# Kernel tuning notes

Measured on AMD Instinct MI355X. Metric: run time of the kernel, lower is better.

## Reference

```python
import jax, jax.numpy as jnp
import numpy as np

D = 192      # model dim (out_channels)
DIN = 384    # d_inner = 2*D
N = 16       # d_state
DTR = 12     # dt_rank = ceil(D/16)
K = 4        # depthwise conv kernel size
NB = 3       # total mamba blocks (2 stacked + 1 in downsample)


def setup_inputs() -> dict:
    key = jax.random.key(0)
    ks = jax.random.split(key, 8)
    rn = lambda k, shape, s: jax.random.normal(k, shape, jnp.float32) * s
    inp = {
        "x": jax.random.normal(ks[0], (2, 96, 56, 56), jnp.float32),
        "proj_w": rn(ks[1], (D, 96), 0.1),
        "proj_b": jnp.zeros((D,), jnp.float32),
        "bn_g": jnp.ones((D,), jnp.float32),
        "bn_b": jnp.zeros((D,), jnp.float32),
        "bn_mean": jnp.zeros((D,), jnp.float32),
        "bn_var": jnp.ones((D,), jnp.float32),
        "ln_g": jnp.ones((NB, D), jnp.float32),
        "ln_b": jnp.zeros((NB, D), jnp.float32),
        "Win": rn(ks[2], (NB, 2 * DIN, D), 0.05),
        "b_in": jnp.zeros((NB, 2 * DIN), jnp.float32),
        "conv_w": rn(ks[3], (NB, DIN, K), 0.2),
        "conv_b": jnp.zeros((NB, DIN), jnp.float32),
        "Wx": rn(ks[4], (NB, DTR + 2 * N, DIN), 0.05),
        "Wdt": rn(ks[5], (NB, DIN, DTR), 0.05),
        "bdt": jnp.full((NB, DIN), -4.6, jnp.float32),  # softplus ~ 0.01
        "A_log": jnp.log(jnp.broadcast_to(jnp.arange(1, N + 1, dtype=jnp.float32), (NB, DIN, N))),
        "Dskip": jnp.ones((NB, DIN), jnp.float32),
        "Wout": rn(ks[6], (NB, D, DIN), 0.05),
        "bout": jnp.zeros((NB, D), jnp.float32),
    }
    return inp


def _mamba(x, ln_g, ln_b, Win, b_in, conv_w, conv_b, Wx, Wdt, bdt, A_log, Dskip, Wout, bout):
    # x: (B, C, H, W) -> flatten spatial dims to a sequence (B, L, C)
    B, C, H, W = x.shape
    L = H * W
    seq = x.reshape(B, C, L).transpose(0, 2, 1)
    mu = seq.mean(-1, keepdims=True)
    var = seq.var(-1, keepdims=True)
    h = (seq - mu) * jax.lax.rsqrt(var + 1e-5) * ln_g + ln_b  # LayerNorm
    xz = jnp.einsum('bld,ed->ble', h, Win) + b_in              # (B, L, 2*DIN)
    xi, z = jnp.split(xz, 2, axis=-1)
    # depthwise causal conv1d along L
    xc = jnp.pad(xi.transpose(0, 2, 1), ((0, 0), (0, 0), (K - 1, 0)))
    xc = jax.lax.conv_general_dilated(xc, conv_w[:, None, :], (1,), 'VALID',
                                      feature_group_count=DIN) + conv_b[:, None]
    xi = jax.nn.silu(xc).transpose(0, 2, 1)                    # (B, L, DIN)
    proj = jnp.einsum('ble,pe->blp', xi, Wx)                   # (B, L, DTR+2N)
    dtl = proj[..., :DTR]
    Bm = proj[..., DTR:DTR + N]
    Cm = proj[..., DTR + N:]
    dt = jax.nn.softplus(jnp.einsum('blr,er->ble', dtl, Wdt) + bdt)  # (B, L, DIN)
    A = -jnp.exp(A_log)                                         # (DIN, N)
    dA = jnp.exp(dt[..., None] * A)                             # (B, L, DIN, N)
    dBx = (dt * xi)[..., None] * Bm[:, :, None, :]              # (B, L, DIN, N)

    def step(hc, t):
        dA_t, dBx_t, C_t = t
        hc = dA_t * hc + dBx_t                                  # (B, DIN, N)
        return hc, jnp.einsum('ben,bn->be', hc, C_t)

    h0 = jnp.zeros((B, DIN, N), x.dtype)
    _, ys = jax.lax.scan(step, h0, (dA.transpose(1, 0, 2, 3),
                                    dBx.transpose(1, 0, 2, 3),
                                    Cm.transpose(1, 0, 2)))
    y = ys.transpose(1, 0, 2) + Dskip * xi
    y = y * jax.nn.silu(z)
    out = jnp.einsum('ble,de->bld', y, Wout) + bout
    return out.transpose(0, 2, 1).reshape(B, C, H, W)


def _maxpool2(x):
    return jax.lax.reduce_window(x, -jnp.inf, jax.lax.max,
                                 (1, 1, 2, 2), (1, 1, 2, 2), 'VALID')


def reference(x, proj_w, proj_b, bn_g, bn_b, bn_mean, bn_var, ln_g, ln_b, Win, b_in,
              conv_w, conv_b, Wx, Wdt, bdt, A_log, Dskip, Wout, bout):
    # proj (conv1x1) + BatchNorm (eval-mode running stats)
    x = jnp.einsum('bchw,oc->bohw', x, proj_w) + proj_b[:, None, None]
    x = (x - bn_mean[:, None, None]) * jax.lax.rsqrt(bn_var[:, None, None] + 1e-5) \
        * bn_g[:, None, None] + bn_b[:, None, None]
    blk = lambda i, v: _mamba(v, ln_g[i], ln_b[i], Win[i], b_in[i], conv_w[i], conv_b[i],
                              Wx[i], Wdt[i], bdt[i], A_log[i], Dskip[i], Wout[i], bout[i])
    for i in range(2):  # residual mamba blocks
        x = x + blk(i, x)
    skip = x
    x = blk(2, _maxpool2(x))  # downsample: maxpool then mamba (no residual)
    return (x, skip)
```

## Files before the change

### kernel.cpp

```cpp
#include <hip/hip_runtime.h>

typedef __attribute__((ext_vector_type(8))) __bf16 bf16x8;
typedef __attribute__((ext_vector_type(4))) __bf16 bf16x4;
typedef __attribute__((ext_vector_type(4))) float f32x4;

#define DEV static __device__ __forceinline__

DEV float fast_rcp(float x) { return __builtin_amdgcn_rcpf(x); }
DEV float sigm(float x) { return fast_rcp(1.f + __expf(-x)); }
DEV float siluf(float x) { return x * sigm(x); }
DEV float softplusf(float x) { return x > 20.f ? x : __logf(1.f + __expf(x)); }


__global__ __launch_bounds__(256) void k_proj_wcvt(
    const float* __restrict__ x, const float* __restrict__ pw,
    const float* __restrict__ pb, const float* __restrict__ bng,
    const float* __restrict__ bnb, const float* __restrict__ bnm,
    const float* __restrict__ bnv, float* __restrict__ v,
    const float* __restrict__ Win, const float* __restrict__ Wout,
    const float* __restrict__ Wx, __bf16* __restrict__ Wb)
{
  constexpr int SAP = 104;
  __shared__ __bf16 As[64 * SAP];
  __shared__ __bf16 Ws[64 * SAP];
  const int tid = threadIdx.x;
  const int bid = blockIdx.x;

  if (bid >= 294) {
    const int idx = ((bid - 294) * 256 + tid) * 4;
    if (idx < 714240) {
      const float* src;
      if (idx < 442368) src = Win + idx;
      else if (idx < 663552) src = Wout + (idx - 442368);
      else src = Wx + (idx - 663552);
      const float4 tv = *(const float4*)src;
      bf16x4 o;
      o[0] = (__bf16)tv.x; o[1] = (__bf16)tv.y;
      o[2] = (__bf16)tv.z; o[3] = (__bf16)tv.w;
      *(bf16x4*)(Wb + idx) = o;
    }
    return;
  }

  const int r0 = (bid % 98) * 64;
  const int col0 = (bid / 98) * 64;
  const int b = r0 / 3136, l0 = r0 % 3136;
  const int lane = tid & 63, wv = tid >> 6;
  const int rh = wv >> 1, ch = wv & 1;
  const int lm = lane & 15, quad = lane >> 4;

#pragma unroll
  for (int it = 0; it < 6; ++it) {
    const int idx = tid + it * 256;
    const int c = idx >> 4, l4 = idx & 15;
    const float4 t = *(const float4*)(x + ((size_t)(b * 96 + c)) * 3136 + l0 + l4 * 4);
    As[(l4 * 4 + 0) * SAP + c] = (__bf16)t.x;
    As[(l4 * 4 + 1) * SAP + c] = (__bf16)t.y;
    As[(l4 * 4 + 2) * SAP + c] = (__bf16)t.z;
    As[(l4 * 4 + 3) * SAP + c] = (__bf16)t.w;
  }
#pragma unroll
  for (int it = 0; it < 6; ++it) {
    const int idx = tid + it * 256;
    const int wr = idx / 24, kc = (idx % 24) * 4;
    const float4 t = *(const float4*)(pw + (size_t)(col0 + wr) * 96 + kc);
    bf16x4 o;
    o[0] = (__bf16)t.x; o[1] = (__bf16)t.y; o[2] = (__bf16)t.z; o[3] = (__bf16)t.w;
    *(bf16x4*)(&Ws[wr * SAP + kc]) = o;
  }
  __syncthreads();

  f32x4 acc[2][2] = {};
#pragma unroll
  for (int ks = 0; ks < 3; ++ks) {
    const int kb = ks * 32 + quad * 8;
    bf16x8 a0 = *(const bf16x8*)(&As[(rh * 32 + lm) * SAP + kb]);
    bf16x8 a1 = *(const bf16x8*)(&As[(rh * 32 + 16 + lm) * SAP + kb]);
    bf16x8 b0 = *(const bf16x8*)(&Ws[(ch * 32 + lm) * SAP + kb]);
    bf16x8 b1 = *(const bf16x8*)(&Ws[(ch * 32 + 16 + lm) * SAP + kb]);
    acc[0][0] = __builtin_amdgcn_mfma_f32_16x16x32_bf16(a0, b0, acc[0][0], 0, 0, 0);
    acc[0][1] = __builtin_amdgcn_mfma_f32_16x16x32_bf16(a0, b1, acc[0][1], 0, 0, 0);
    acc[1][0] = __builtin_amdgcn_mfma_f32_16x16x32_bf16(a1, b0, acc[1][0], 0, 0, 0);
    acc[1][1] = __builtin_amdgcn_mfma_f32_16x16x32_bf16(a1, b1, acc[1][1], 0, 0, 0);
  }

#pragma unroll
  for (int ti = 0; ti < 2; ++ti)
#pragma unroll
    for (int tj = 0; tj < 2; ++tj) {
      const int gcol = col0 + ch * 32 + tj * 16 + lm;
      const float s = rsqrtf(bnv[gcol] + 1e-5f) * bng[gcol];
      const float sh = (pb[gcol] - bnm[gcol]) * s + bnb[gcol];
#pragma unroll
      for (int j = 0; j < 4; ++j) {
        const int grow = r0 + rh * 32 + ti * 16 + quad * 4 + j;
        v[(size_t)grow * 192 + gcol] = acc[ti][tj][j] * s + sh;
      }
    }
}

__global__ __launch_bounds__(256) void k_conv(
    const float* __restrict__ xz, __bf16* __restrict__ xiB,
    const float* __restrict__ cw, const float* __restrict__ cb,
    int Lseq, int nthreads)
{
  const int idx = blockIdx.x * 256 + threadIdx.x;
  if (idx >= nthreads) return;
  const int e = idx % 384;
  const int seg = idx / 384;
  const int nseg = Lseq / 8;
  const int b = seg / nseg;
  const int l0 = (seg % nseg) * 8;
  const float4 w4 = *(const float4*)(cw + e * 4);
  const float bv = cb[e];
  float xv[11];
#pragma unroll
  for (int k = 0; k < 11; ++k) {
    const int l = l0 - 3 + k;
    xv[k] = (l >= 0) ? xz[(size_t)(b * Lseq + l) * 768 + e] : 0.f;
  }
#pragma unroll
  for (int j = 0; j < 8; ++j) {
    const float a = bv + xv[j] * w4.x + xv[j + 1] * w4.y + xv[j + 2] * w4.z + xv[j + 3] * w4.w;
    xiB[(size_t)(b * Lseq + l0 + j) * 384 + e] = (__bf16)siluf(a);
  }
}

template <int AMODE>
__global__ __launch_bounds__(256, 4) void k_gemm_xz(
    const float* __restrict__ A, const __bf16* __restrict__ W,
    const float* __restrict__ bias, float* __restrict__ O,
    int M, const float* __restrict__ lng, const float* __restrict__ lnb)
{
  constexpr int SA = 200;
  __shared__ __bf16 As[64 * SA];
  __shared__ float lnS[384];
  const int tid = threadIdx.x;
  const int r0 = blockIdx.x * 64;
  const int col0 = blockIdx.y * 128;
  const int lane = tid & 63, wv = tid >> 6;
  const int rh = wv & 1, ch = wv >> 1;
  const int lm = lane & 15, quad = lane >> 4;

  if (tid < 192) { lnS[tid] = lng[tid]; lnS[192 + tid] = lnb[tid]; }
  __syncthreads();

  {
    const int row = tid >> 2, part = tid & 3;
    const int gr = min(r0 + row, M - 1);
    const int cbase = part * 48;
    float4 tv[12];
    if constexpr (AMODE == 2) {
#pragma unroll
      for (int j = 0; j < 12; ++j)
        tv[j] = *(const float4*)(A + (size_t)gr * 192 + cbase + j * 4);
    } else {
      const int bb = gr / 784, l2 = gr % 784;
      const int h2 = l2 / 28, w2 = l2 % 28;
      const float* p0 = A + (size_t)(bb * 3136 + h2 * 112 + w2 * 2) * 192;
#pragma unroll
      for (int j = 0; j < 12; ++j) {
        const int cc = cbase + j * 4;
        const float4 a0 = *(const float4*)(p0 + cc);
        const float4 a1 = *(const float4*)(p0 + 192 + cc);
        const float4 a2 = *(const float4*)(p0 + 56 * 192 + cc);
        const float4 a3 = *(const float4*)(p0 + 57 * 192 + cc);
        tv[j].x = fmaxf(fmaxf(a0.x, a1.x), fmaxf(a2.x, a3.x));
        tv[j].y = fmaxf(fmaxf(a0.y, a1.y), fmaxf(a2.y, a3.y));
        tv[j].z = fmaxf(fmaxf(a0.z, a1.z), fmaxf(a2.z, a3.z));
        tv[j].w = fmaxf(fmaxf(a0.w, a1.w), fmaxf(a2.w, a3.w));
      }
    }
    float s = 0.f, sq = 0.f;
#pragma unroll
    for (int j = 0; j < 12; ++j) {
      s += tv[j].x + tv[j].y + tv[j].z + tv[j].w;
      sq += tv[j].x * tv[j].x + tv[j].y * tv[j].y + tv[j].z * tv[j].z + tv[j].w * tv[j].w;
    }
    s += __shfl_xor(s, 1); s += __shfl_xor(s, 2);
    sq += __shfl_xor(sq, 1); sq += __shfl_xor(sq, 2);
    const float mean = s * (1.f / 192.f);
    const float rstd = rsqrtf(sq * (1.f / 192.f) - mean * mean + 1e-5f);
#pragma unroll
    for (int j = 0; j < 12; ++j) {
      const int c = cbase + j * 4;
      bf16x4 o;
      o[0] = (__bf16)((tv[j].x - mean) * rstd * lnS[c + 0] + lnS[192 + c + 0]);
      o[1] = (__bf16)((tv[j].y - mean) * rstd * lnS[c + 1] + lnS[192 + c + 1]);
      o[2] = (__bf16)((tv[j].z - mean) * rstd * lnS[c + 2] + lnS[192 + c + 2]);
      o[3] = (__bf16)((tv[j].w - mean) * rstd * lnS[c + 3] + lnS[192 + c + 3]);
      *(bf16x4*)(&As[row * SA + c]) = o;
    }
  }
  __syncthreads();

  f32x4 acc[2][4] = {};
#pragma unroll
  for (int ks = 0; ks < 6; ++ks) {
    const int kb = ks * 32 + quad * 8;
    bf16x8 a0 = *(const bf16x8*)(&As[(rh * 32 + lm) * SA + kb]);
    bf16x8 a1 = *(const bf16x8*)(&As[(rh * 32 + 16 + lm) * SA + kb]);
#pragma unroll
    for (int tj = 0; tj < 4; ++tj) {
      const int gw = col0 + ch * 64 + tj * 16 + lm;
      bf16x8 bfr = *(const bf16x8*)(W + (size_t)gw * 192 + kb);
      acc[0][tj] = __builtin_amdgcn_mfma_f32_16x16x32_bf16(a0, bfr, acc[0][tj], 0, 0, 0);
      acc[1][tj] = __builtin_amdgcn_mfma_f32_16x16x32_bf16(a1, bfr, acc[1][tj], 0, 0, 0);
    }
  }

#pragma unroll
  for (int ti = 0; ti < 2; ++ti)
#pragma unroll
    for (int tj = 0; tj < 4; ++tj) {
      const int gcol = col0 + ch * 64 + tj * 16 + lm;
      const float bv = bias[gcol];
#pragma unroll
      for (int j = 0; j < 4; ++j) {
        const int rowt = rh * 32 + ti * 16 + quad * 4 + j;
        const int grow = r0 + rowt;
        if (grow < M) O[(size_t)grow * 768 + gcol] = acc[ti][tj][j] + bv;
      }
    }
}

constexpr int EPI_G2 = 1, EPI_RES = 2, EPI_RES_SKIP = 3, EPI_OUT2 = 4;

template <int EPI>
__global__ __launch_bounds__(256) void k_gemm_s(
    const __bf16* __restrict__ Ab, const __bf16* __restrict__ W,
    const float* __restrict__ bias, float* __restrict__ O,
    int M, int K, int Nvalid,
    float* __restrict__ dtlbuf, float* __restrict__ bcbuf,
    float* __restrict__ oflt)
{
  constexpr int SA = 200;
  __shared__ __bf16 As[16 * SA];
  __shared__ float dtlS[(EPI == EPI_G2) ? 16 * 12 : 1];
  const int tid = threadIdx.x;
  const int r0 = blockIdx.x * 16;
  const int col0 = blockIdx.y * 64;
  const int lane = tid & 63, wv = tid >> 6;
  const int ch = wv;
  const int lm = lane & 15, quad = lane >> 4;

  f32x4 acc = {};
  const int nkp = K / 192;
  for (int kp = 0; kp < nkp; ++kp) {
    if (kp) __syncthreads();
    {
      const int idx = tid;
      const int row = idx / 24, kc = (idx % 24) * 8;
      const int gr = min(r0 + row, M - 1);
      if (row < 16)
        *(bf16x8*)(&As[row * SA + kc]) =
            *(const bf16x8*)(Ab + (size_t)gr * K + kp * 192 + kc);
      const int idx2 = tid + 256;
      if (idx2 < 384) {
        const int row2 = idx2 / 24, kc2 = (idx2 % 24) * 8;
        const int gr2 = min(r0 + row2, M - 1);
        *(bf16x8*)(&As[row2 * SA + kc2]) =
            *(const bf16x8*)(Ab + (size_t)gr2 * K + kp * 192 + kc2);
      }
    }
    __syncthreads();
#pragma unroll
    for (int ks = 0; ks < 6; ++ks) {
      const int kb = ks * 32 + quad * 8;
      bf16x8 a0 = *(const bf16x8*)(&As[lm * SA + kb]);
      const int gw = min(col0 + ch * 16 + lm, Nvalid - 1);
      bf16x8 bfr = *(const bf16x8*)(W + (size_t)gw * K + kp * 192 + kb);
      acc = __builtin_amdgcn_mfma_f32_16x16x32_bf16(a0, bfr, acc, 0, 0, 0);
    }
  }

  const int colt = ch * 16 + lm;
  if constexpr (EPI == EPI_G2) {
#pragma unroll
    for (int j = 0; j < 4; ++j) {
      const int rowt = quad * 4 + j;
      const int grow = r0 + rowt;
      const float val = acc[j];
      if (colt < 12) dtlS[rowt * 12 + colt] = val;
      else if (colt < 44 && grow < M)
        bcbuf[(size_t)grow * 32 + (colt - 12)] = val;
    }
    __syncthreads();
    if (tid < 192) {
      const int grow = r0 + tid / 12;
      if (grow < M) dtlbuf[(size_t)grow * 12 + tid % 12] = dtlS[tid];
    }
  } else {
    const int gcol = col0 + colt;
    const float bv = bias[gcol];
#pragma unroll
    for (int j = 0; j < 4; ++j) {
      const int rowt = quad * 4 + j;
      const int grow = r0 + rowt;
      if (grow >= M) continue;
      const float val = acc[j] + bv;
      if constexpr (EPI == EPI_RES) {
        O[(size_t)grow * 192 + gcol] += val;
      } else if constexpr (EPI == EPI_RES_SKIP) {
        const float nv = O[(size_t)grow * 192 + gcol] + val;
        O[(size_t)grow * 192 + gcol] = nv;
        const int b = grow / 3136, l = grow % 3136;
        oflt[b * 602112 + gcol * 3136 + l] = nv;
      } else {
        const int b = grow / 784, l = grow % 784;
        oflt[b * 150528 + gcol * 784 + l] = val;
      }
    }
  }
}

constexpr int SC_LC = 14, SC_T = 7, SC_TN = 2;

DEV void compute_dts(const float* __restrict__ dtl, const float* __restrict__ Wdt,
                     const float* __restrict__ bdt, int rowbase, int e, int t,
                     float* dtlS, float* wdtS)
{
  for (int idx = t; idx < SC_LC * 12; idx += 128)
    dtlS[idx] = dtl[(size_t)(rowbase + idx / 12) * 12 + idx % 12];
#pragma unroll
  for (int r = 0; r < 12; ++r) wdtS[r * 128 + t] = Wdt[(size_t)e * 12 + r];
}

__global__ __launch_bounds__(128) void k_scan1(
    const float* __restrict__ dtl, const __bf16* __restrict__ xi,
    const float* __restrict__ bc, const float* __restrict__ Wdt,
    const float* __restrict__ bdt, const float* __restrict__ A_log,
    float* __restrict__ DT, float* __restrict__ S, int Lseq, int NC)
{
  __shared__ float Bs[SC_LC * 16];
  __shared__ float dts[SC_LC * 128];
  __shared__ float dtlS[SC_LC * 12];
  __shared__ float wdtS[12 * 128];
  const int t = threadIdx.x;
  const int e = blockIdx.y * 128 + t;
  const int c = blockIdx.x % NC;
  const int b = blockIdx.x / NC;
  const int rowbase = b * Lseq + c * SC_LC;

  for (int idx = t; idx < SC_LC * 16; idx += 128) {
    const int l = idx >> 4, q = idx & 15;
    Bs[idx] = bc[(size_t)(rowbase + l) * 32 + q];
  }
  compute_dts(dtl, Wdt, bdt, rowbase, e, t, dtlS, wdtS);
  const float bdte = bdt[e];

  float An2[16];
  {
    const float4* a4 = (const float4*)(A_log + e * 16);
    float4 t0 = a4[0], t1 = a4[1], t2 = a4[2], t3 = a4[3];
    float tmp[16] = {t0.x, t0.y, t0.z, t0.w, t1.x, t1.y, t1.z, t1.w,
                     t2.x, t2.y, t2.z, t2.w, t3.x, t3.y, t3.z, t3.w};
#pragma unroll
    for (int n = 0; n < 16; ++n) An2[n] = -__expf(tmp[n]) * 1.44269504f;
  }
  __syncthreads();
  float dtsum = 0.f;
  for (int l = 0; l < SC_LC; ++l) {
    float a = bdte;
#pragma unroll
    for (int r = 0; r < 12; ++r) a += dtlS[l * 12 + r] * wdtS[r * 128 + t];
    const float sp = softplusf(a);
    dts[l * 128 + t] = sp;
    dtsum += sp;
  }

  float h[16];
#pragma unroll
  for (int n = 0; n < 16; ++n) h[n] = 0.f;

  float xA[SC_T], xB[SC_T];
  auto LOADA = [&](int tt) {
#pragma unroll
    for (int j = 0; j < SC_T; ++j)
      xA[j] = (float)xi[(size_t)(rowbase + tt * SC_T + j) * 384 + e];
  };
  auto LOADB = [&](int tt) {
#pragma unroll
    for (int j = 0; j < SC_T; ++j)
      xB[j] = (float)xi[(size_t)(rowbase + tt * SC_T + j) * 384 + e];
  };
  auto COMP = [&](const float (&x8)[SC_T], int tt) {
#pragma unroll
    for (int j = 0; j < SC_T; ++j) {
      const int l = tt * SC_T + j;
      const float dtv = dts[l * 128 + t];
      const float u = dtv * x8[j];
      const float* Brow = &Bs[l * 16];
#pragma unroll
      for (int n = 0; n < 16; ++n) {
        const float a = __builtin_amdgcn_exp2f(dtv * An2[n]);
        h[n] = a * h[n] + u * Brow[n];
      }
    }
  };

  LOADA(0);
#pragma unroll
  for (int tt = 0; tt < SC_TN; ++tt) {
    if (tt & 1) { if (tt + 1 < SC_TN) LOADA(tt + 1); COMP(xB, tt); }
    else        { if (tt + 1 < SC_TN) LOADB(tt + 1); COMP(xA, tt); }
  }

  const size_t o = ((size_t)(b * NC + c) * 384 + e) * 16;
#pragma unroll
  for (int q = 0; q < 4; ++q)
    *(float4*)(S + o + q * 4) = make_float4(h[q*4], h[q*4+1], h[q*4+2], h[q*4+3]);
  DT[(size_t)(b * NC + c) * 384 + e] = dtsum;
}

__global__ __launch_bounds__(256) void k_carry(
    const float* __restrict__ DT, float* __restrict__ SH,
    const float* __restrict__ A_log, int NC)
{
  const int tid = blockIdx.x * 256 + threadIdx.x;
  const int b = tid / 6144, r = tid % 6144;
  const float An2 = -__expf(A_log[r]) * 1.44269504f;
  const size_t o = (size_t)b * NC * 6144 + r;
  const size_t od = (size_t)b * NC * 384 + (r >> 4);

  float sA[8], dA[8], sB[8], dB[8];
  auto LOAD = [&](float (&sv)[8], float (&dv)[8], int c0) {
#pragma unroll
    for (int k = 0; k < 8; ++k) {
      sv[k] = SH[o + (size_t)(c0 + k) * 6144];
      dv[k] = DT[od + (size_t)(c0 + k) * 384];
    }
  };
  float h = 0.f;
  auto COMP = [&](const float (&sv)[8], const float (&dv)[8], int c0) {
    float a[8];
#pragma unroll
    for (int k = 0; k < 8; ++k) a[k] = __builtin_amdgcn_exp2f(An2 * dv[k]);
#pragma unroll
    for (int k = 0; k < 8; ++k) {
      SH[o + (size_t)(c0 + k) * 6144] = h;
      h = a[k] * h + sv[k];
    }
  };

  LOAD(sA, dA, 0);
  for (int c0 = 0; c0 < NC; c0 += 16) {
    if (c0 + 8 < NC) LOAD(sB, dB, c0 + 8);
    COMP(sA, dA, c0);
    if (c0 + 8 < NC) {
      if (c0 + 16 < NC) LOAD(sA, dA, c0 + 16);
      COMP(sB, dB, c0 + 8);
    }
  }
}

__global__ __launch_bounds__(128) void k_scan2(
    const float* __restrict__ dtl, const __bf16* __restrict__ xi,
    const float* __restrict__ bc, const float* __restrict__ xz,
    const float* __restrict__ Wdt, const float* __restrict__ bdt,
    const float* __restrict__ A_log, const float* __restrict__ Dskip,
    const float* __restrict__ H0, __bf16* __restrict__ y, int Lseq, int NC)
{
  __shared__ float BCs[SC_LC * 32];
  __shared__ float dts[SC_LC * 128];
  __shared__ float dtlS[SC_LC * 12];
  __shared__ float wdtS[12 * 128];
  const int t = threadIdx.x;
  const int e = blockIdx.y * 128 + t;
  const int c = blockIdx.x % NC;
  const int b = blockIdx.x / NC;
  const int rowbase = b * Lseq + c * SC_LC;

  for (int idx = t; idx < SC_LC * 32; idx += 128)
    BCs[idx] = bc[(size_t)rowbase * 32 + idx];
  compute_dts(dtl, Wdt, bdt, rowbase, e, t, dtlS, wdtS);
  const float bdte = bdt[e];

  float An2[16];
  {
    const float4* a4 = (const float4*)(A_log + e * 16);
    float4 t0 = a4[0], t1 = a4[1], t2 = a4[2], t3 = a4[3];
    float tmp[16] = {t0.x, t0.y, t0.z, t0.w, t1.x, t1.y, t1.z, t1.w,
                     t2.x, t2.y, t2.z, t2.w, t3.x, t3.y, t3.z, t3.w};
#pragma unroll
    for (int n = 0; n < 16; ++n) An2[n] = -__expf(tmp[n]) * 1.44269504f;
  }
  float h[16];
  {
    const size_t o = ((size_t)(b * NC + c) * 384 + e) * 16;
    const float4* h4 = (const float4*)(H0 + o);
    float4 t0 = h4[0], t1 = h4[1], t2 = h4[2], t3 = h4[3];
    h[0]=t0.x; h[1]=t0.y; h[2]=t0.z; h[3]=t0.w;
    h[4]=t1.x; h[5]=t1.y; h[6]=t1.z; h[7]=t1.w;
    h[8]=t2.x; h[9]=t2.y; h[10]=t2.z; h[11]=t2.w;
    h[12]=t3.x; h[13]=t3.y; h[14]=t3.z; h[15]=t3.w;
  }
  __syncthreads();
  for (int l = 0; l < SC_LC; ++l) {
    float a = bdte;
#pragma unroll
    for (int r = 0; r < 12; ++r) a += dtlS[l * 12 + r] * wdtS[r * 128 + t];
    dts[l * 128 + t] = softplusf(a);
  }
  const float Dse = Dskip[e];

  float xA[SC_T], zA[SC_T], xB[SC_T], zB[SC_T];
  auto LOADA = [&](int tt) {
#pragma unroll
    for (int j = 0; j < SC_T; ++j) {
      const size_t r = (size_t)(rowbase + tt * SC_T + j);
      xA[j] = (float)xi[r * 384 + e];
      zA[j] = xz[r * 768 + 384 + e];
    }
  };
  auto LOADB = [&](int tt) {
#pragma unroll
    for (int j = 0; j < SC_T; ++j) {
      const size_t r = (size_t)(rowbase + tt * SC_T + j);
      xB[j] = (float)xi[r * 384 + e];
      zB[j] = xz[r * 768 + 384 + e];
    }
  };
  auto COMP = [&](const float (&x8)[SC_T], const float (&z8)[SC_T], int tt) {
#pragma unroll
    for (int j = 0; j < SC_T; ++j) {
      const int l = tt * SC_T + j;
      const float dtv = dts[l * 128 + t];
      const float xiv = x8[j];
      const float u = dtv * xiv;
      const float* Brow = &BCs[l * 32];
      const float* Crow = Brow + 16;
      float yv = 0.f;
#pragma unroll
      for (int n = 0; n < 16; ++n) {
        const float a = __builtin_amdgcn_exp2f(dtv * An2[n]);
        h[n] = a * h[n] + u * Brow[n];
        yv += h[n] * Crow[n];
      }
      y[(size_t)(rowbase + l) * 384 + e] = (__bf16)((yv + Dse * xiv) * siluf(z8[j]));
    }
  };

  LOADA(0);
#pragma unroll
  for (int tt = 0; tt < SC_TN; ++tt) {
    if (tt & 1) { if (tt + 1 < SC_TN) LOADA(tt + 1); COMP(xB, zB, tt); }
    else        { if (tt + 1 < SC_TN) LOADB(tt + 1); COMP(xA, zA, tt); }
  }
}

extern "C" void kernel_launch(void* const* d_in, const int* in_sizes, int n_in,
                              void* d_out, int out_size, void* d_ws, size_t ws_size,
                              hipStream_t stream)
{
  const float* x    = (const float*)d_in[0];
  const float* pw   = (const float*)d_in[1];
  const float* pb   = (const float*)d_in[2];
  const float* bng  = (const float*)d_in[3];
  const float* bnb  = (const float*)d_in[4];
  const float* bnm  = (const float*)d_in[5];
  const float* bnv  = (const float*)d_in[6];
  const float* lng  = (const float*)d_in[7];
  const float* lnb  = (const float*)d_in[8];
  const float* Win  = (const float*)d_in[9];
  const float* b_in = (const float*)d_in[10];
  const float* cw   = (const float*)d_in[11];
  const float* cb   = (const float*)d_in[12];
  const float* Wx   = (const float*)d_in[13];
  const float* Wdt  = (const float*)d_in[14];
  const float* bdt  = (const float*)d_in[15];
  const float* Alog = (const float*)d_in[16];
  const float* Dsk  = (const float*)d_in[17];
  const float* Wout = (const float*)d_in[18];
  const float* bout = (const float*)d_in[19];

  float* wsf = (float*)d_ws;
  float* v    = wsf;
  float* xz   = v + 1204224;
  float* dtlb = xz + 4816896;
  float* bcb  = dtlb + 75264;
  float* Sb   = bcb + 200704;
  float* Pb   = Sb + 2752512;
  __bf16* xiB = (__bf16*)(Pb + 2752512);
  __bf16* yB  = (__bf16*)(Pb + 2752512 + 1204224);
  __bf16* Wb  = (__bf16*)(Pb + 2752512 + 2408448);

  float* out0 = (float*)d_out;
  float* out1 = out0 + 301056;

  k_proj_wcvt<<<992, 256, 0, stream>>>(x, pw, pb, bng, bnb, bnm, bnv, v,
                                       Win, Wout, Wx, Wb);

  for (int i = 0; i < 3; ++i) {
    const int big = (i < 2) ? 1 : 0;
    const int Lseq = big ? 3136 : 784;
    const int M = 2 * Lseq;
    const int NC = Lseq / SC_LC;
    const int MB = (M + 63) / 64;
    const int MB16 = M / 16;
    const float* lng_i = lng + i * 192;
    const float* lnb_i = lnb + i * 192;
    const float* bin_i = b_in + i * 768;
    const float* cw_i  = cw + i * 384 * 4;
    const float* cb_i  = cb + i * 384;
    const float* Wdt_i = Wdt + i * 384 * 12;
    const float* bdt_i = bdt + i * 384;
    const float* Al_i  = Alog + i * 384 * 16;
    const float* Ds_i  = Dsk + i * 384;
    const float* bo_i  = bout + i * 192;
    const __bf16* Winb_i  = Wb + i * 147456;
    const __bf16* Woutb_i = Wb + 442368 + i * 73728;
    const __bf16* Wxb_i   = Wb + 663552 + i * 16896;

    if (big)
      k_gemm_xz<2><<<dim3(MB, 6), 256, 0, stream>>>(
          v, Winb_i, bin_i, xz, M, lng_i, lnb_i);
    else
      k_gemm_xz<3><<<dim3(MB, 6), 256, 0, stream>>>(
          v, Winb_i, bin_i, xz, M, lng_i, lnb_i);
    k_conv<<<(M * 384 / 8 + 255) / 256, 256, 0, stream>>>(
        xz, xiB, cw_i, cb_i, Lseq, M * 384 / 8);
    k_gemm_s<EPI_G2><<<dim3(MB16, 1), 256, 0, stream>>>(
        xiB, Wxb_i, nullptr, nullptr, M, 384, 44, dtlb, bcb, nullptr);
    k_scan1<<<dim3(2 * NC, 3), 128, 0, stream>>>(
        dtlb, xiB, bcb, Wdt_i, bdt_i, Al_i, Pb, Sb, Lseq, NC);
    k_carry<<<48, 256, 0, stream>>>(Pb, Sb, Al_i, NC);
    k_scan2<<<dim3(2 * NC, 3), 128, 0, stream>>>(
        dtlb, xiB, bcb, xz, Wdt_i, bdt_i, Al_i, Ds_i, Sb, yB, Lseq, NC);
    if (i == 0)
      k_gemm_s<EPI_RES><<<dim3(MB16, 3), 256, 0, stream>>>(
          yB, Woutb_i, bo_i, v, M, 384, 192, nullptr, nullptr, nullptr);
    else if (i == 1)
      k_gemm_s<EPI_RES_SKIP><<<dim3(MB16, 3), 256, 0, stream>>>(
          yB, Woutb_i, bo_i, v, M, 384, 192, nullptr, nullptr, out1);
    else
      k_gemm_s<EPI_OUT2><<<dim3(MB16, 3), 256, 0, stream>>>(
          yB, Woutb_i, bo_i, v, M, 384, 192, nullptr, nullptr, out0);
  }
}
```

Baseline: 346.1 us.

## Split each channel's 16-state scan across two threads in scan kernels

Both chunked scan kernels now run 256 threads per block, with each channel's 16 state elements split into two halves of 8 handled by adjacent threads. The dt softplus precompute is also split across the pair, and partial sums and y outputs are combined with a lane shuffle. The Wdt staging is loaded cooperatively and all x/z values for the chunk are loaded up front instead of double-buffered. This doubles thread-level parallelism and halves per-thread register state, at the cost of redundant x loads, an extra barrier and a shuffle per step.

```diff
diff --git a/kernel.cpp b/kernel.cpp
--- a/kernel.cpp
+++ b/kernel.cpp
@@ -314,19 +314,9 @@
   }
 }
 
-constexpr int SC_LC = 14, SC_T = 7, SC_TN = 2;
-
-DEV void compute_dts(const float* __restrict__ dtl, const float* __restrict__ Wdt,
-                     const float* __restrict__ bdt, int rowbase, int e, int t,
-                     float* dtlS, float* wdtS)
-{
-  for (int idx = t; idx < SC_LC * 12; idx += 128)
-    dtlS[idx] = dtl[(size_t)(rowbase + idx / 12) * 12 + idx % 12];
-#pragma unroll
-  for (int r = 0; r < 12; ++r) wdtS[r * 128 + t] = Wdt[(size_t)e * 12 + r];
-}
-
-__global__ __launch_bounds__(128) void k_scan1(
+constexpr int SC_LC = 14;
+
+__global__ __launch_bounds__(256) void k_scan1(
     const float* __restrict__ dtl, const __bf16* __restrict__ xi,
     const float* __restrict__ bc, const float* __restrict__ Wdt,
     const float* __restrict__ bdt, const float* __restrict__ A_log,
@@ -337,80 +327,69 @@
   __shared__ float dtlS[SC_LC * 12];
   __shared__ float wdtS[12 * 128];
   const int t = threadIdx.x;
-  const int e = blockIdx.y * 128 + t;
+  const int el = t >> 1, half = t & 1, n0h = half * 8;
+  const int e0 = blockIdx.y * 128;
+  const int e = e0 + el;
   const int c = blockIdx.x % NC;
   const int b = blockIdx.x / NC;
   const int rowbase = b * Lseq + c * SC_LC;
 
-  for (int idx = t; idx < SC_LC * 16; idx += 128) {
-    const int l = idx >> 4, q = idx & 15;
-    Bs[idx] = bc[(size_t)(rowbase + l) * 32 + q];
-  }
-  compute_dts(dtl, Wdt, bdt, rowbase, e, t, dtlS, wdtS);
+  if (t < SC_LC * 16)
+    Bs[t] = bc[(size_t)(rowbase + (t >> 4)) * 32 + (t & 15)];
+  if (t < SC_LC * 12)
+    dtlS[t] = dtl[(size_t)(rowbase + t / 12) * 12 + t % 12];
+  for (int idx = t; idx < 12 * 128; idx += 256) {
+    const int r = idx >> 7, ee = idx & 127;
+    wdtS[idx] = Wdt[(size_t)(e0 + ee) * 12 + r];
+  }
   const float bdte = bdt[e];
 
-  float An2[16];
+  float An2[8];
   {
-    const float4* a4 = (const float4*)(A_log + e * 16);
-    float4 t0 = a4[0], t1 = a4[1], t2 = a4[2], t3 = a4[3];
-    float tmp[16] = {t0.x, t0.y, t0.z, t0.w, t1.x, t1.y, t1.z, t1.w,
-                     t2.x, t2.y, t2.z, t2.w, t3.x, t3.y, t3.z, t3.w};
-#pragma unroll
-    for (int n = 0; n < 16; ++n) An2[n] = -__expf(tmp[n]) * 1.44269504f;
+    const float4* a4 = (const float4*)(A_log + e * 16 + n0h);
+    float4 t0 = a4[0], t1 = a4[1];
+    float tmp[8] = {t0.x, t0.y, t0.z, t0.w, t1.x, t1.y, t1.z, t1.w};
+#pragma unroll
+    for (int n = 0; n < 8; ++n) An2[n] = -__expf(tmp[n]) * 1.44269504f;
   }
   __syncthreads();
-  float dtsum = 0.f;
+  float dtp = 0.f;
+#pragma unroll
+  for (int j = 0; j < 7; ++j) {
+    const int l = half * 7 + j;
+    float a = bdte;
+#pragma unroll
+    for (int r = 0; r < 12; ++r) a += dtlS[l * 12 + r] * wdtS[r * 128 + el];
+    const float sp = softplusf(a);
+    dts[l * 128 + el] = sp;
+    dtp += sp;
+  }
+  const float dtsum = dtp + __shfl_xor(dtp, 1);
+  __syncthreads();
+
+  float xall[SC_LC];
+#pragma unroll
+  for (int l = 0; l < SC_LC; ++l)
+    xall[l] = (float)xi[(size_t)(rowbase + l) * 384 + e];
+
+  float h[8];
+#pragma unroll
+  for (int n = 0; n < 8; ++n) h[n] = 0.f;
+#pragma unroll
   for (int l = 0; l < SC_LC; ++l) {
-    float a = bdte;
-#pragma unroll
-    for (int r = 0; r < 12; ++r) a += dtlS[l * 12 + r] * wdtS[r * 128 + t];
-    const float sp = softplusf(a);
-    dts[l * 128 + t] = sp;
-    dtsum += sp;
-  }
-
-  float h[16];
-#pragma unroll
-  for (int n = 0; n < 16; ++n) h[n] = 0.f;
-
-  float xA[SC_T], xB[SC_T];
-  auto LOADA = [&](int tt) {
-#pragma unroll
-    for (int j = 0; j < SC_T; ++j)
-      xA[j] = (float)xi[(size_t)(rowbase + tt * SC_T + j) * 384 + e];
-  };
-  auto LOADB = [&](int tt) {
-#pragma unroll
-    for (int j = 0; j < SC_T; ++j)
-      xB[j] = (float)xi[(size_t)(rowbase + tt * SC_T + j) * 384 + e];
-  };
-  auto COMP = [&](const float (&x8)[SC_T], int tt) {
-#pragma unroll
-    for (int j = 0; j < SC_T; ++j) {
-      const int l = tt * SC_T + j;
-      const float dtv = dts[l * 128 + t];
-      const float u = dtv * x8[j];
-      const float* Brow = &Bs[l * 16];
-#pragma unroll
-      for (int n = 0; n < 16; ++n) {
-        const float a = __builtin_amdgcn_exp2f(dtv * An2[n]);
-        h[n] = a * h[n] + u * Brow[n];
-      }
-    }
-  };
-
-  LOADA(0);
-#pragma unroll
-  for (int tt = 0; tt < SC_TN; ++tt) {
-    if (tt & 1) { if (tt + 1 < SC_TN) LOADA(tt + 1); COMP(xB, tt); }
-    else        { if (tt + 1 < SC_TN) LOADB(tt + 1); COMP(xA, tt); }
-  }
-
-  const size_t o = ((size_t)(b * NC + c) * 384 + e) * 16;
-#pragma unroll
-  for (int q = 0; q < 4; ++q)
-    *(float4*)(S + o + q * 4) = make_float4(h[q*4], h[q*4+1], h[q*4+2], h[q*4+3]);
-  DT[(size_t)(b * NC + c) * 384 + e] = dtsum;
+    const float dtv = dts[l * 128 + el];
+    const float u = dtv * xall[l];
+    const float* Brow = &Bs[l * 16 + n0h];
+#pragma unroll
+    for (int n = 0; n < 8; ++n) {
+      const float a = __builtin_amdgcn_exp2f(dtv * An2[n]);
+      h[n] = a * h[n] + u * Brow[n];
+    }
+  }
+  const size_t o = ((size_t)(b * NC + c) * 384 + e) * 16 + n0h;
+  *(float4*)(S + o)     = make_float4(h[0], h[1], h[2], h[3]);
+  *(float4*)(S + o + 4) = make_float4(h[4], h[5], h[6], h[7]);
+  if (half == 0) DT[(size_t)(b * NC + c) * 384 + e] = dtsum;
 }
 
 __global__ __launch_bounds__(256) void k_carry(
@@ -454,7 +433,7 @@
   }
 }
 
-__global__ __launch_bounds__(128) void k_scan2(
+__global__ __launch_bounds__(256) void k_scan2(
     const float* __restrict__ dtl, const __bf16* __restrict__ xi,
     const float* __restrict__ bc, const float* __restrict__ xz,
     const float* __restrict__ Wdt, const float* __restrict__ bdt,
@@ -466,86 +445,76 @@
   __shared__ float dtlS[SC_LC * 12];
   __shared__ float wdtS[12 * 128];
   const int t = threadIdx.x;
-  const int e = blockIdx.y * 128 + t;
+  const int el = t >> 1, half = t & 1, n0h = half * 8;
+  const int e0 = blockIdx.y * 128;
+  const int e = e0 + el;
   const int c = blockIdx.x % NC;
   const int b = blockIdx.x / NC;
   const int rowbase = b * Lseq + c * SC_LC;
 
-  for (int idx = t; idx < SC_LC * 32; idx += 128)
+  for (int idx = t; idx < SC_LC * 32; idx += 256)
     BCs[idx] = bc[(size_t)rowbase * 32 + idx];
-  compute_dts(dtl, Wdt, bdt, rowbase, e, t, dtlS, wdtS);
+  if (t < SC_LC * 12)
+    dtlS[t] = dtl[(size_t)(rowbase + t / 12) * 12 + t % 12];
+  for (int idx = t; idx < 12 * 128; idx += 256) {
+    const int r = idx >> 7, ee = idx & 127;
+    wdtS[idx] = Wdt[(size_t)(e0 + ee) * 12 + r];
+  }
   const float bdte = bdt[e];
 
-  float An2[16];
+  float An2[8];
   {
-    const float4* a4 = (const float4*)(A_log + e * 16);
-    float4 t0 = a4[0], t1 = a4[1], t2 = a4[2], t3 = a4[3];
-    float tmp[16] = {t0.x, t0.y, t0.z, t0.w, t1.x, t1.y, t1.z, t1.w,
-                     t2.x, t2.y, t2.z, t2.w, t3.x, t3.y, t3.z, t3.w};
-#pragma unroll
-    for (int n = 0; n < 16; ++n) An2[n] = -__expf(tmp[n]) * 1.44269504f;
-  }
-  float h[16];
+    const float4* a4 = (const float4*)(A_log + e * 16 + n0h);
+    float4 t0 = a4[0], t1 = a4[1];
+    float tmp[8] = {t0.x, t0.y, t0.z, t0.w, t1.x, t1.y, t1.z, t1.w};
+#pragma unroll
+    for (int n = 0; n < 8; ++n) An2[n] = -__expf(tmp[n]) * 1.44269504f;
+  }
+  float h[8];
   {
-    const size_t o = ((size_t)(b * NC + c) * 384 + e) * 16;
+    const size_t o = ((size_t)(b * NC + c) * 384 + e) * 16 + n0h;
     const float4* h4 = (const float4*)(H0 + o);
-    float4 t0 = h4[0], t1 = h4[1], t2 = h4[2], t3 = h4[3];
+    float4 t0 = h4[0], t1 = h4[1];
     h[0]=t0.x; h[1]=t0.y; h[2]=t0.z; h[3]=t0.w;
     h[4]=t1.x; h[5]=t1.y; h[6]=t1.z; h[7]=t1.w;
-    h[8]=t2.x; h[9]=t2.y; h[10]=t2.z; h[11]=t2.w;
-    h[12]=t3.x; h[13]=t3.y; h[14]=t3.z; h[15]=t3.w;
   }
   __syncthreads();
+#pragma unroll
+  for (int j = 0; j < 7; ++j) {
+    const int l = half * 7 + j;
+    float a = bdte;
+#pragma unroll
+    for (int r = 0; r < 12; ++r) a += dtlS[l * 12 + r] * wdtS[r * 128 + el];
+    dts[l * 128 + el] = softplusf(a);
+  }
+  __syncthreads();
+  const float Dse = Dskip[e];
+
+  float xall[SC_LC], zall[SC_LC];
+#pragma unroll
   for (int l = 0; l < SC_LC; ++l) {
-    float a = bdte;
-#pragma unroll
-    for (int r = 0; r < 12; ++r) a += dtlS[l * 12 + r] * wdtS[r * 128 + t];
-    dts[l * 128 + t] = softplusf(a);
-  }
-  const float Dse = Dskip[e];
-
-  float xA[SC_T], zA[SC_T], xB[SC_T], zB[SC_T];
-  auto LOADA = [&](int tt) {
-#pragma unroll
-    for (int j = 0; j < SC_T; ++j) {
-      const size_t r = (size_t)(rowbase + tt * SC_T + j);
-      xA[j] = (float)xi[r * 384 + e];
-      zA[j] = xz[r * 768 + 384 + e];
-    }
-  };
-  auto LOADB = [&](int tt) {
-#pragma unroll
-    for (int j = 0; j < SC_T; ++j) {
-      const size_t r = (size_t)(rowbase + tt * SC_T + j);
-      xB[j] = (float)xi[r * 384 + e];
-      zB[j] = xz[r * 768 + 384 + e];
-    }
-  };
-  auto COMP = [&](const float (&x8)[SC_T], const float (&z8)[SC_T], int tt) {
-#pragma unroll
-    for (int j = 0; j < SC_T; ++j) {
-      const int l = tt * SC_T + j;
-      const float dtv = dts[l * 128 + t];
-      const float xiv = x8[j];
-      const float u = dtv * xiv;
-      const float* Brow = &BCs[l * 32];
-      const float* Crow = Brow + 16;
-      float yv = 0.f;
-#pragma unroll
-      for (int n = 0; n < 16; ++n) {
-        const float a = __builtin_amdgcn_exp2f(dtv * An2[n]);
-        h[n] = a * h[n] + u * Brow[n];
-        yv += h[n] * Crow[n];
-      }
-      y[(size_t)(rowbase + l) * 384 + e] = (__bf16)((yv + Dse * xiv) * siluf(z8[j]));
-    }
-  };
-
-  LOADA(0);
-#pragma unroll
-  for (int tt = 0; tt < SC_TN; ++tt) {
-    if (tt & 1) { if (tt + 1 < SC_TN) LOADA(tt + 1); COMP(xB, zB, tt); }
-    else        { if (tt + 1 < SC_TN) LOADB(tt + 1); COMP(xA, zA, tt); }
+    const size_t r = (size_t)(rowbase + l);
+    xall[l] = (float)xi[r * 384 + e];
+    zall[l] = xz[r * 768 + 384 + e];
+  }
+
+#pragma unroll
+  for (int l = 0; l < SC_LC; ++l) {
+    const float dtv = dts[l * 128 + el];
+    const float xiv = xall[l];
+    const float u = dtv * xiv;
+    const float* Brow = &BCs[l * 32 + n0h];
+    const float* Crow = &BCs[l * 32 + 16 + n0h];
+    float yv = 0.f;
+#pragma unroll
+    for (int n = 0; n < 8; ++n) {
+      const float a = __builtin_amdgcn_exp2f(dtv * An2[n]);
+      h[n] = a * h[n] + u * Brow[n];
+      yv += h[n] * Crow[n];
+    }
+    const float yt = yv + __shfl_xor(yv, 1);
+    if (half == 0)
+      y[(size_t)(rowbase + l) * 384 + e] = (__bf16)((yt + Dse * xiv) * siluf(zall[l]));
   }
 }
 
@@ -622,10 +591,10 @@
         xz, xiB, cw_i, cb_i, Lseq, M * 384 / 8);
     k_gemm_s<EPI_G2><<<dim3(MB16, 1), 256, 0, stream>>>(
         xiB, Wxb_i, nullptr, nullptr, M, 384, 44, dtlb, bcb, nullptr);
-    k_scan1<<<dim3(2 * NC, 3), 128, 0, stream>>>(
+    k_scan1<<<dim3(2 * NC, 3), 256, 0, stream>>>(
         dtlb, xiB, bcb, Wdt_i, bdt_i, Al_i, Pb, Sb, Lseq, NC);
     k_carry<<<48, 256, 0, stream>>>(Pb, Sb, Al_i, NC);
-    k_scan2<<<dim3(2 * NC, 3), 128, 0, stream>>>(
+    k_scan2<<<dim3(2 * NC, 3), 256, 0, stream>>>(
         dtlb, xiB, bcb, xz, Wdt_i, bdt_i, Al_i, Ds_i, Sb, yB, Lseq, NC);
     if (i == 0)
       k_gemm_s<EPI_RES><<<dim3(MB16, 3), 256, 0, stream>>>(
```

New measurement: 335.0 us. -3.2%, faster.
